# Optimization experiments

Hardware: AMD Instinct MI355X
Metric: run time of the kernel (lower is better)

## Reference

```python
import jax, jax.numpy as jnp
import numpy as np

IGNORE_INDEX = 255
BOUNDARY_WEIGHT = 2.0


def setup_inputs() -> dict:
    key = jax.random.key(0)
    k1, k2 = jax.random.split(key)
    inputs = jax.random.normal(k1, (8, 21, 512, 512), dtype=jnp.float32)
    targets = jax.random.randint(k2, (8, 512, 512), 0, 21, dtype=jnp.int64)
    return {"inputs": inputs, "targets": targets}


def _boundary_map(targets):
    # Faithful to the original loops: for each interior (i, j), take the 3x3
    # patch over ALL batches; compute max-min over the ROW axis (dim=1) per
    # column; if ANY entry (across batch and the 3 columns) differs, mark
    # (i, j) as boundary for ALL batch elements.
    t = targets
    # row-wise (vertical) 3-tap max/min over rows i-1, i, i+1 -> (B, H-2, W)
    rmax = jnp.maximum(jnp.maximum(t[:, :-2, :], t[:, 1:-1, :]), t[:, 2:, :])
    rmin = jnp.minimum(jnp.minimum(t[:, :-2, :], t[:, 1:-1, :]), t[:, 2:, :])
    diff = (rmax - rmin) > 0  # (B, H-2, W)
    # any over the 3 patch columns j-1, j, j+1 -> (B, H-2, W-2)
    cany = diff[:, :, :-2] | diff[:, :, 1:-1] | diff[:, :, 2:]
    # any over batch (the original `.any()` reduces over everything)
    bmap = jnp.any(cany, axis=0)  # (H-2, W-2)
    boundary = jnp.zeros(t.shape, dtype=jnp.float32)
    boundary = boundary.at[:, 1:-1, 1:-1].set(
        jnp.broadcast_to(bmap.astype(jnp.float32), (t.shape[0],) + bmap.shape)
    )
    return boundary


def reference(inputs, targets):
    # per-pixel cross entropy with ignore_index (reduction='none' -> 0 at ignored)
    logp = jax.nn.log_softmax(inputs, axis=1)  # (B, C, H, W)
    valid = targets != IGNORE_INDEX
    safe_t = jnp.where(valid, targets, 0)
    ce = -jnp.take_along_axis(logp, safe_t[:, None, :, :], axis=1)[:, 0]  # (B,H,W)
    ce = jnp.where(valid, ce, 0.0)
    boundary = _boundary_map(targets)
    weighted = ce * (1.0 + BOUNDARY_WEIGHT * boundary)
    return weighted.mean()
```

## Files before the change

kernel.cpp:

```cpp
#include <hip/hip_runtime.h>

#define BATCH 8
#define NCLS 21
#define H 512
#define W 512
#define IGNORE_INDEX 255
#define HW (H * W)
#define NPIX (BATCH * H * W)

__global__ void zero_out_kernel(float* out) {
    if (threadIdx.x == 0 && blockIdx.x == 0) out[0] = 0.0f;
}

__global__ void boundary_kernel(const int* __restrict__ t,
                                unsigned char* __restrict__ bmap) {
    int idx = blockIdx.x * blockDim.x + threadIdx.x;
    if (idx >= HW) return;
    int h = idx / W;
    int w = idx % W;
    unsigned char bd = 0;
    if (h > 0 && h < H - 1 && w > 0 && w < W - 1) {
        for (int b = 0; b < BATCH && !bd; ++b) {
            const int* base = t + b * HW;
            #pragma unroll
            for (int dw = -1; dw <= 1; ++dw) {
                int ww = w + dw;
                int a = base[(h - 1) * W + ww];
                int m = base[h * W + ww];
                int c = base[(h + 1) * W + ww];
                if ((a != m) | (m != c)) { bd = 1; break; }
            }
        }
    }
    bmap[idx] = bd;
}

__global__ __launch_bounds__(256)
void ce_kernel(const float* __restrict__ x, const int* __restrict__ t,
               const unsigned char* __restrict__ bmap,
               float* __restrict__ out) {
    float local = 0.0f;
    const int stride = gridDim.x * blockDim.x;
    for (int idx = blockIdx.x * blockDim.x + threadIdx.x; idx < NPIX;
         idx += stride) {
        int b = idx / HW;
        int hw = idx - b * HW;
        const float* p = x + (size_t)b * NCLS * HW + hw;

        int tg = t[idx];
        bool valid = (tg != IGNORE_INDEX);
        int st = valid ? tg : 0;

        float v[NCLS];
        #pragma unroll
        for (int c = 0; c < NCLS; ++c) v[c] = p[(size_t)c * HW];

        float m = v[0];
        #pragma unroll
        for (int c = 1; c < NCLS; ++c) m = fmaxf(m, v[c]);

        float s = 0.0f;
        float xt = v[0];
        #pragma unroll
        for (int c = 0; c < NCLS; ++c) {
            s += __expf(v[c] - m);
            if (c == st) xt = v[c];
        }
        float ce = __logf(s) + m - xt;
        ce = valid ? ce : 0.0f;

        float wgt = 1.0f + 2.0f * (float)bmap[hw];
        local += ce * wgt;
    }

    #pragma unroll
    for (int off = 32; off > 0; off >>= 1)
        local += __shfl_down(local, off, 64);

    __shared__ float smem[4];
    int lane = threadIdx.x & 63;
    int wave = threadIdx.x >> 6;
    if (lane == 0) smem[wave] = local;
    __syncthreads();
    if (threadIdx.x == 0) {
        float bsum = smem[0] + smem[1] + smem[2] + smem[3];
        atomicAdd(out, bsum * (1.0f / (float)NPIX));
    }
}

extern "C" void kernel_launch(void* const* d_in, const int* in_sizes, int n_in,
                              void* d_out, int out_size, void* d_ws, size_t ws_size,
                              hipStream_t stream) {
    const float* x = (const float*)d_in[0];
    const int* t = (const int*)d_in[1];
    float* out = (float*)d_out;
    unsigned char* bmap = (unsigned char*)d_ws;

    zero_out_kernel<<<1, 64, 0, stream>>>(out);

    boundary_kernel<<<(HW + 255) / 256, 256, 0, stream>>>(t, bmap);

    ce_kernel<<<2048, 256, 0, stream>>>(x, t, bmap, out);
}
```

Before: 248.8 us.

## Vectorize CE kernel to float4 per thread and fold zeroing into boundary kernel

The CE kernel now has each thread process four consecutive pixels with float4 loads of every class plane, int4 target loads and uchar4 boundary loads. The grid-stride loop is replaced by a grid with exactly one thread per four pixels. Zeroing the output moves into the boundary kernel, removing one launch, and the index math uses shifts. The goal is wider memory transactions and less launch overhead, at the cost of four times more live registers (84 floats), which may cut occupancy, and 2048 blocks each issuing an atomic.

```diff
diff --git a/kernel.cpp b/kernel.cpp
--- a/kernel.cpp
+++ b/kernel.cpp
@@ -8,16 +8,14 @@
 #define HW (H * W)
 #define NPIX (BATCH * H * W)
 
-__global__ void zero_out_kernel(float* out) {
-    if (threadIdx.x == 0 && blockIdx.x == 0) out[0] = 0.0f;
-}
-
 __global__ void boundary_kernel(const int* __restrict__ t,
-                                unsigned char* __restrict__ bmap) {
+                                unsigned char* __restrict__ bmap,
+                                float* __restrict__ out) {
     int idx = blockIdx.x * blockDim.x + threadIdx.x;
+    if (idx == 0) out[0] = 0.0f;
     if (idx >= HW) return;
-    int h = idx / W;
-    int w = idx % W;
+    int h = idx >> 9;
+    int w = idx & (W - 1);
     unsigned char bd = 0;
     if (h > 0 && h < H - 1 && w > 0 && w < W - 1) {
         for (int b = 0; b < BATCH && !bd; ++b) {
@@ -35,43 +33,47 @@
     bmap[idx] = bd;
 }
 
+__device__ __forceinline__ float ce_one(const float* __restrict__ v, int tg,
+                                        unsigned int bd) {
+    bool valid = (tg != IGNORE_INDEX);
+    int st = valid ? tg : 0;
+    float m = v[0];
+    #pragma unroll
+    for (int c = 1; c < NCLS; ++c) m = fmaxf(m, v[c]);
+    float s = 0.0f;
+    float xt = v[0];
+    #pragma unroll
+    for (int c = 0; c < NCLS; ++c) {
+        s += __expf(v[c] - m);
+        if (c == st) xt = v[c];
+    }
+    float ce = __logf(s) + m - xt;
+    ce = valid ? ce : 0.0f;
+    return ce * (1.0f + 2.0f * (float)bd);
+}
+
 __global__ __launch_bounds__(256)
 void ce_kernel(const float* __restrict__ x, const int* __restrict__ t,
                const unsigned char* __restrict__ bmap,
                float* __restrict__ out) {
-    float local = 0.0f;
-    const int stride = gridDim.x * blockDim.x;
-    for (int idx = blockIdx.x * blockDim.x + threadIdx.x; idx < NPIX;
-         idx += stride) {
-        int b = idx / HW;
-        int hw = idx - b * HW;
-        const float* p = x + (size_t)b * NCLS * HW + hw;
+    int tid = blockIdx.x * blockDim.x + threadIdx.x;
+    int idx4 = tid << 2;
+    int b = idx4 >> 18;
+    int hw = idx4 & (HW - 1);
+    const float* p = x + (size_t)b * NCLS * HW + hw;
 
-        int tg = t[idx];
-        bool valid = (tg != IGNORE_INDEX);
-        int st = valid ? tg : 0;
+    int4 tg = *(const int4*)(t + idx4);
+    uchar4 bm = *(const uchar4*)(bmap + hw);
 
-        float v[NCLS];
-        #pragma unroll
-        for (int c = 0; c < NCLS; ++c) v[c] = p[(size_t)c * HW];
+    float v0[NCLS], v1[NCLS], v2[NCLS], v3[NCLS];
+    #pragma unroll
+    for (int c = 0; c < NCLS; ++c) {
+        float4 q = *(const float4*)(p + (size_t)c * HW);
+        v0[c] = q.x; v1[c] = q.y; v2[c] = q.z; v3[c] = q.w;
+    }
 
-        float m = v[0];
-        #pragma unroll
-        for (int c = 1; c < NCLS; ++c) m = fmaxf(m, v[c]);
-
-        float s = 0.0f;
-        float xt = v[0];
-        #pragma unroll
-        for (int c = 0; c < NCLS; ++c) {
-            s += __expf(v[c] - m);
-            if (c == st) xt = v[c];
-        }
-        float ce = __logf(s) + m - xt;
-        ce = valid ? ce : 0.0f;
-
-        float wgt = 1.0f + 2.0f * (float)bmap[hw];
-        local += ce * wgt;
-    }
+    float local = ce_one(v0, tg.x, bm.x) + ce_one(v1, tg.y, bm.y) +
+                  ce_one(v2, tg.z, bm.z) + ce_one(v3, tg.w, bm.w);
 
     #pragma unroll
     for (int off = 32; off > 0; off >>= 1)
@@ -96,9 +98,6 @@
     float* out = (float*)d_out;
     unsigned char* bmap = (unsigned char*)d_ws;
 
-    zero_out_kernel<<<1, 64, 0, stream>>>(out);
-
-    boundary_kernel<<<(HW + 255) / 256, 256, 0, stream>>>(t, bmap);
-
-    ce_kernel<<<2048, 256, 0, stream>>>(x, t, bmap, out);
+    boundary_kernel<<<(HW + 255) / 256, 256, 0, stream>>>(t, bmap, out);
+    ce_kernel<<<NPIX / 4 / 256, 256, 0, stream>>>(x, t, bmap, out);
 }
```

After: 244.9 us. About the same (-1.6%).
